# Kernel optimization log

Hardware: AMD Instinct MI355X
Metric: run time of the kernel (lower is better)

## Reference

```python
import jax, jax.numpy as jnp
import numpy as np

N, CIN, C, L = 6144, 6, 128, 3
SIGMA = 0.3

def _ln(x, g, b, eps=1e-5):
    m = x.mean(-1, keepdims=True)
    v = x.var(-1, keepdims=True)
    return (x - m) / jnp.sqrt(v + eps) * g + b

def _cdist(a):
    n2 = jnp.sum(a * a, -1)
    d2 = n2[:, None] + n2[None, :] - 2.0 * (a @ a.T)
    return jnp.sqrt(jnp.maximum(d2, 0.0))

def setup_inputs():
    key = jax.random.key(0)
    ks = jax.random.split(key, 24)
    s = 1.0 / np.sqrt(C)
    ref = jax.random.normal(ks[0], (N, 3), dtype=jnp.float32)
    src = ref + 0.05 * jax.random.normal(ks[1], (N, 3), dtype=jnp.float32)
    return {
        "ref_keypts": ref,
        "src_keypts": src,
        "corr_feat": jax.random.normal(ks[2], (N, CIN), dtype=jnp.float32),
        "W_in": jax.random.normal(ks[3], (CIN + 6, C), dtype=jnp.float32) * (1.0 / np.sqrt(CIN + 6)),
        "b_in": jnp.zeros((C,), jnp.float32),
        "mlp_W": jax.random.normal(ks[4], (L, C, C), dtype=jnp.float32) * s,
        "mlp_b": jnp.zeros((L, C), jnp.float32),
        "mlp_g": jnp.ones((L, C), jnp.float32),
        "mlp_beta": jnp.zeros((L, C), jnp.float32),
        "Wq": jax.random.normal(ks[5], (L, C, C), dtype=jnp.float32) * s,
        "bq": jnp.zeros((L, C), jnp.float32),
        "Wk": jax.random.normal(ks[6], (L, C, C), dtype=jnp.float32) * s,
        "bk": jnp.zeros((L, C), jnp.float32),
        "Wv": jax.random.normal(ks[7], (L, C, C), dtype=jnp.float32) * s,
        "bv": jnp.zeros((L, C), jnp.float32),
        "Wo": jax.random.normal(ks[8], (L, C, C), dtype=jnp.float32) * s,
        "bo": jnp.zeros((L, C), jnp.float32),
        "ln_g": jnp.ones((L, C), jnp.float32),
        "ln_b": jnp.zeros((L, C), jnp.float32),
        "c1_W": jax.random.normal(ks[9], (C, 32), dtype=jnp.float32) * s,
        "c1_b": jnp.zeros((32,), jnp.float32),
        "c2_W": jax.random.normal(ks[10], (32, 32), dtype=jnp.float32) * (1.0 / np.sqrt(32)),
        "c2_b": jnp.zeros((32,), jnp.float32),
        "c3_W": jax.random.normal(ks[11], (32, 1), dtype=jnp.float32) * (1.0 / np.sqrt(32)),
        "c3_b": jnp.zeros((1,), jnp.float32),
    }

def reference(ref_keypts, src_keypts, corr_feat, W_in, b_in, mlp_W, mlp_b, mlp_g, mlp_beta, Wq, bq, Wk, bk, Wv, bv, Wo, bo, ln_g, ln_b, c1_W, c1_b, c2_W, c2_b, c3_W, c3_b):
    # keypoint-diff embedding
    kp = jnp.concatenate([ref_keypts, src_keypts], -1)          # [N, 6]
    kp = kp - kp.mean(-1, keepdims=True)
    feat = jnp.concatenate([corr_feat, kp], -1) @ W_in + b_in   # [N, C]
    # geometric compatibility (no grad in original -> stop_gradient)
    geo = _cdist(ref_keypts) - _cdist(src_keypts)               # [N, N]
    geo = jnp.maximum(1.0 - geo * geo / (SIGMA * SIGMA), 0.0)
    geo = jax.lax.stop_gradient(geo)
    scale = 1.0 / np.sqrt(C)
    for i in range(L):
        # UnaryBlock: Linear -> norm -> LeakyReLU(0.1)
        h = _ln(feat @ mlp_W[i] + mlp_b[i], mlp_g[i], mlp_beta[i])
        feat = jnp.where(h > 0, h, 0.1 * h)
        # AttentionLayer (1 head) with multiplicative attention_factors
        q = feat @ Wq[i] + bq[i]
        k = feat @ Wk[i] + bk[i]
        v = feat @ Wv[i] + bv[i]
        attn = jax.nn.softmax(geo * ((q @ k.T) * scale), axis=-1)  # [N, N]
        hid = (attn @ v) @ Wo[i] + bo[i]
        feat = _ln(hid + feat, ln_g[i], ln_b[i])
    feat = feat / jnp.maximum(jnp.linalg.norm(feat, axis=-1, keepdims=True), 1e-12)
    h = jax.nn.relu(feat @ c1_W + c1_b)
    h = jax.nn.relu(h @ c2_W + c2_b)
    score = jax.nn.sigmoid(h @ c3_W + c3_b)[:, 0]
    return feat, score
```

## Files before the change

kernel.cpp:

```cpp
#include <hip/hip_runtime.h>
#include <math.h>

#define NPTS 6144
#define CH   128

typedef __attribute__((ext_vector_type(8))) short short8;
typedef __attribute__((ext_vector_type(4))) float f32x4;
typedef __attribute__((ext_vector_type(2))) float f32x2;
typedef __attribute__((ext_vector_type(4))) int   i32x4;

__device__ inline ushort f2bf(float f) {
  union { float f; unsigned u; } v; v.f = f;
  unsigned u = v.u;
  u += 0x7fff + ((u >> 16) & 1);
  return (ushort)(u >> 16);
}

__device__ inline f32x2 splat2(float x) { return (f32x2){x, x}; }

__device__ inline float fsqrt(float x) {
  float r; asm("v_sqrt_f32 %0, %1" : "=v"(r) : "v"(x)); return r;
}
__device__ inline float fexp2(float x) {
  float r; asm("v_exp_f32 %0, %1" : "=v"(r) : "v"(x)); return r;
}
__device__ inline unsigned cvtpk(float a, float b) {
  unsigned r;
  asm("v_cvt_pk_bf16_f32 %0, %1, %2" : "=v"(r) : "v"(a), "v"(b));
  return r;
}

__global__ __launch_bounds__(128) void k_embed(
    const float* __restrict__ refp, const float* __restrict__ srcp,
    const float* __restrict__ cf, const float* __restrict__ Win,
    const float* __restrict__ bin, float* __restrict__ out) {
  const int row = blockIdx.x, j = threadIdx.x;
  __shared__ float inb[12];
  __shared__ float mkp;
  if (j < 6)       inb[j] = cf[row * 6 + j];
  else if (j < 9)  inb[j] = refp[row * 3 + (j - 6)];
  else if (j < 12) inb[j] = srcp[row * 3 + (j - 9)];
  __syncthreads();
  if (j == 0) {
    float s = inb[6] + inb[7] + inb[8] + inb[9] + inb[10] + inb[11];
    mkp = s * (1.0f / 6.0f);
  }
  __syncthreads();
  float acc = bin[j];
  #pragma unroll
  for (int kk = 0; kk < 12; kk++) {
    float x = inb[kk] - (kk >= 6 ? mkp : 0.0f);
    acc = fmaf(x, Win[kk * CH + j], acc);
  }
  out[row * CH + j] = acc;
}

__global__ __launch_bounds__(128) void k_mlp_qkv(
    const float* __restrict__ X, const float* __restrict__ W,
    const float* __restrict__ b, const float* __restrict__ g,
    const float* __restrict__ beta,
    const float* __restrict__ Wq, const float* __restrict__ bq,
    const float* __restrict__ Wk, const float* __restrict__ bk,
    const float* __restrict__ Wv, const float* __restrict__ bv,
    float* __restrict__ T, ushort* __restrict__ Q, ushort* __restrict__ K,
    ushort* __restrict__ Vt) {
  const int j = threadIdx.x;
  const int r0 = blockIdx.x * 4;
  __shared__ float xs[4][CH];
  __shared__ float hs[4][CH];
  __shared__ float red[2][4];
  #pragma unroll
  for (int r = 0; r < 4; r++) xs[r][j] = X[(r0 + r) * CH + j];
  __syncthreads();

  float acc[4];
  const float bj = b[j];
  #pragma unroll
  for (int r = 0; r < 4; r++) acc[r] = bj;
  for (int kk = 0; kk < CH; kk++) {
    float wv_ = W[kk * CH + j];
    #pragma unroll
    for (int r = 0; r < 4; r++) acc[r] = fmaf(xs[r][kk], wv_, acc[r]);
  }
  const int wv2 = j >> 6, ln = j & 63;
  float sum[4];
  #pragma unroll
  for (int r = 0; r < 4; r++) sum[r] = acc[r];
  #pragma unroll
  for (int o = 32; o; o >>= 1) {
    #pragma unroll
    for (int r = 0; r < 4; r++) sum[r] += __shfl_xor(sum[r], o);
  }
  if (ln == 0) {
    #pragma unroll
    for (int r = 0; r < 4; r++) red[wv2][r] = sum[r];
  }
  __syncthreads();
  float dv[4];
  #pragma unroll
  for (int r = 0; r < 4; r++) {
    float mean = (red[0][r] + red[1][r]) * (1.0f / 128.0f);
    dv[r] = acc[r] - mean;
    sum[r] = dv[r] * dv[r];
  }
  #pragma unroll
  for (int o = 32; o; o >>= 1) {
    #pragma unroll
    for (int r = 0; r < 4; r++) sum[r] += __shfl_xor(sum[r], o);
  }
  __syncthreads();
  if (ln == 0) {
    #pragma unroll
    for (int r = 0; r < 4; r++) red[wv2][r] = sum[r];
  }
  __syncthreads();
  const float gj = g[j], betaj = beta[j];
  #pragma unroll
  for (int r = 0; r < 4; r++) {
    float var = (red[0][r] + red[1][r]) * (1.0f / 128.0f);
    float y = dv[r] * rsqrtf(var + 1e-5f) * gj + betaj;
    y = (y > 0.0f) ? y : 0.1f * y;
    T[(r0 + r) * CH + j] = y;
    hs[r][j] = y;
  }
  __syncthreads();

  float aq[4], ak[4], av[4];
  const float bqj = bq[j], bkj = bk[j], bvj = bv[j];
  #pragma unroll
  for (int r = 0; r < 4; r++) { aq[r] = bqj; ak[r] = bkj; av[r] = bvj; }
  for (int kk = 0; kk < CH; kk++) {
    float wq = Wq[kk * CH + j], wk = Wk[kk * CH + j], wv_ = Wv[kk * CH + j];
    #pragma unroll
    for (int r = 0; r < 4; r++) {
      float x = hs[r][kk];
      aq[r] = fmaf(x, wq, aq[r]);
      ak[r] = fmaf(x, wk, ak[r]);
      av[r] = fmaf(x, wv_, av[r]);
    }
  }
  const float scale = 0.12751879524143007f;
  #pragma unroll
  for (int r = 0; r < 4; r++) {
    Q[(r0 + r) * CH + j] = f2bf(aq[r] * scale);
    K[(r0 + r) * CH + j] = f2bf(ak[r]);
  }
  ushort4 vp;
  vp.x = f2bf(av[0]); vp.y = f2bf(av[1]); vp.z = f2bf(av[2]); vp.w = f2bf(av[3]);
  const int w0 = r0 & 63;
  const int pos = (r0 & ~63) + 32 * ((w0 >> 5) & 1) + 8 * ((w0 >> 2) & 3) +
                  4 * ((w0 >> 4) & 1);
  *(ushort4*)(Vt + (size_t)j * NPTS + pos) = vp;
}

__global__ __launch_bounds__(256, 2) void k_attn_mfma(
    const ushort* __restrict__ Q, const ushort* __restrict__ K,
    const ushort* __restrict__ Vt,
    const float* __restrict__ refp, const float* __restrict__ srcp,
    float* __restrict__ Opart, float* __restrict__ ML, int ntiles) {
  const int tid = threadIdx.x;
  const int w = tid >> 6, ln = tid & 63;
  const int l15 = ln & 15, g = ln >> 4;
  const int row0 = blockIdx.x * 128;
  const int seg = blockIdx.y;
  const int t0 = seg * ntiles;

  __shared__ ushort Ks[64][128];
  __shared__ ushort Vs[128][64];
  __shared__ float cs2[6][64];

  int kofs[4], vofs[4];
  size_t kgo[4], vgo[4];
  #pragma unroll
  for (int s = 0; s < 4; s++) {
    int idx = tid + 256 * s;
    int kr = idx >> 4, kc = idx & 15;
    kofs[s] = kr * 256 + (((kc ^ (kr & 7)) << 4));
    kgo[s] = (size_t)kr * CH + kc * 8;
    int vr = idx >> 3, vc = idx & 7;
    vofs[s] = vr * 128 + (((vc ^ (vr & 7)) << 4));
    vgo[s] = (size_t)vr * NPTS + vc * 8;
  }

  short8 kreg[4], vreg[4];
  float cr[6];

  auto issue = [&](int t) {
    #pragma unroll
    for (int s = 0; s < 4; s++) {
      kreg[s] = *(const short8*)(K + (size_t)(t * 64) * CH + kgo[s]);
      vreg[s] = *(const short8*)(Vt + vgo[s] + t * 64);
    }
    if (tid < 64) {
      int gj = t * 64 + tid;
      cr[0] = refp[gj * 3]; cr[1] = refp[gj * 3 + 1]; cr[2] = refp[gj * 3 + 2];
      cr[3] = srcp[gj * 3]; cr[4] = srcp[gj * 3 + 1]; cr[5] = srcp[gj * 3 + 2];
    }
  };

  const int qbase = row0 + 32 * w;
  const int q1 = qbase + l15, q2 = qbase + 16 + l15;
  short8 qfA[4], qfB[4];
  {
    const ushort* qpA = Q + (size_t)q1 * CH + 8 * g;
    const ushort* qpB = Q + (size_t)q2 * CH + 8 * g;
    #pragma unroll
    for (int ks = 0; ks < 4; ks++) {
      qfA[ks] = *(const short8*)(qpA + 32 * ks);
      qfB[ks] = *(const short8*)(qpB + 32 * ks);
    }
  }
  const float rq10 = refp[q1 * 3], rq11 = refp[q1 * 3 + 1], rq12 = refp[q1 * 3 + 2];
  const float sq10 = srcp[q1 * 3], sq11 = srcp[q1 * 3 + 1], sq12 = srcp[q1 * 3 + 2];
  const float rq20 = refp[q2 * 3], rq21 = refp[q2 * 3 + 1], rq22 = refp[q2 * 3 + 2];
  const float sq20 = srcp[q2 * 3], sq21 = srcp[q2 * 3 + 1], sq22 = srcp[q2 * 3 + 2];

  f32x4 oA[8], oB[8];
  #pragma unroll
  for (int n = 0; n < 8; n++) {
    oA[n] = (f32x4){0.f, 0.f, 0.f, 0.f};
    oB[n] = (f32x4){0.f, 0.f, 0.f, 0.f};
  }
  float m1 = -1e30f, l1 = 0.0f, m2 = -1e30f, l2 = 0.0f;
  const float invs2 = 1.0f / (0.3f * 0.3f);

  issue(t0);
  #pragma unroll
  for (int s = 0; s < 4; s++) {
    *(short8*)((char*)&Ks[0][0] + kofs[s]) = kreg[s];
    *(short8*)((char*)&Vs[0][0] + vofs[s]) = vreg[s];
  }
  if (tid < 64) {
    #pragma unroll
    for (int d = 0; d < 6; d++) cs2[d][tid] = cr[d];
  }
  __syncthreads();

  for (int tt = 0; tt < ntiles; tt++) {
    if (tt + 1 < ntiles) issue(t0 + tt + 1);

    f32x4 accA[4], accB[4];
    #pragma unroll
    for (int nb = 0; nb < 4; nb++) {
      accA[nb] = (f32x4){0.f, 0.f, 0.f, 0.f};
      accB[nb] = (f32x4){0.f, 0.f, 0.f, 0.f};
    }
    __builtin_amdgcn_s_setprio(1);
    #pragma unroll
    for (int ks = 0; ks < 4; ks++) {
      #pragma unroll
      for (int nb = 0; nb < 4; nb++) {
        const char* src = (const char*)&Ks[0][0] + (16 * nb + l15) * 256 +
                          (((4 * ks + g) ^ (l15 & 7)) << 4);
        short8 af = *(const short8*)src;
        accA[nb] = __builtin_amdgcn_mfma_f32_16x16x32_bf16(af, qfA[ks], accA[nb], 0, 0, 0);
        accB[nb] = __builtin_amdgcn_mfma_f32_16x16x32_bf16(af, qfB[ks], accB[nb], 0, 0, 0);
      }
    }
    __builtin_amdgcn_s_setprio(0);

    float pA[4][4], pB[4][4];
    #pragma unroll
    for (int nb = 0; nb < 4; nb++) {
      const int kb = 16 * nb + 4 * g;
      #pragma unroll
      for (int pp = 0; pp < 2; pp++) {
        const int k2 = kb + 2 * pp;
        f32x2 cx = *(const f32x2*)&cs2[0][k2];
        f32x2 cy = *(const f32x2*)&cs2[1][k2];
        f32x2 cz = *(const f32x2*)&cs2[2][k2];
        f32x2 sx = *(const f32x2*)&cs2[3][k2];
        f32x2 sy = *(const f32x2*)&cs2[4][k2];
        f32x2 sz = *(const f32x2*)&cs2[5][k2];
        {
          f32x2 dx = splat2(rq10) - cx, dy = splat2(rq11) - cy, dz = splat2(rq12) - cz;
          f32x2 d2r = dx * dx + dy * dy + dz * dz;
          dx = splat2(sq10) - sx; dy = splat2(sq11) - sy; dz = splat2(sq12) - sz;
          f32x2 d2s = dx * dx + dy * dy + dz * dz;
          f32x2 prod = d2r * d2s, sum2 = d2r + d2s;
          float s0 = fsqrt(prod[0]), s1 = fsqrt(prod[1]);
          float dd20 = fmaf(-2.0f, s0, sum2[0]);
          float dd21 = fmaf(-2.0f, s1, sum2[1]);
          float gg0 = fmaxf(fmaf(dd20, -invs2, 1.0f), 0.0f);
          float gg1 = fmaxf(fmaf(dd21, -invs2, 1.0f), 0.0f);
          pA[nb][2 * pp]     = gg0 * accA[nb][2 * pp];
          pA[nb][2 * pp + 1] = gg1 * accA[nb][2 * pp + 1];
        }
        {
          f32x2 dx = splat2(rq20) - cx, dy = splat2(rq21) - cy, dz = splat2(rq22) - cz;
          f32x2 d2r = dx * dx + dy * dy + dz * dz;
          dx = splat2(sq20) - sx; dy = splat2(sq21) - sy; dz = splat2(sq22) - sz;
          f32x2 d2s = dx * dx + dy * dy + dz * dz;
          f32x2 prod = d2r * d2s, sum2 = d2r + d2s;
          float s0 = fsqrt(prod[0]), s1 = fsqrt(prod[1]);
          float dd20 = fmaf(-2.0f, s0, sum2[0]);
          float dd21 = fmaf(-2.0f, s1, sum2[1]);
          float gg0 = fmaxf(fmaf(dd20, -invs2, 1.0f), 0.0f);
          float gg1 = fmaxf(fmaf(dd21, -invs2, 1.0f), 0.0f);
          pB[nb][2 * pp]     = gg0 * accB[nb][2 * pp];
          pB[nb][2 * pp + 1] = gg1 * accB[nb][2 * pp + 1];
        }
      }
    }

    float tm1 = pA[0][0], tm2 = pB[0][0];
    #pragma unroll
    for (int nb = 0; nb < 4; nb++)
      #pragma unroll
      for (int r = 0; r < 4; r++) {
        tm1 = fmaxf(tm1, pA[nb][r]);
        tm2 = fmaxf(tm2, pB[nb][r]);
      }
    tm1 = fmaxf(tm1, __shfl_xor(tm1, 16));
    tm1 = fmaxf(tm1, __shfl_xor(tm1, 32));
    tm2 = fmaxf(tm2, __shfl_xor(tm2, 16));
    tm2 = fmaxf(tm2, __shfl_xor(tm2, 32));
    if (__any((tm1 > m1 + 11.0f) || (tm2 > m2 + 11.0f))) {
      float nm1 = fmaxf(m1, tm1), nm2 = fmaxf(m2, tm2);
      float rs1 = fexp2(m1 - nm1), rs2 = fexp2(m2 - nm2);
      l1 *= rs1; l2 *= rs2;
      #pragma unroll
      for (int n = 0; n < 8; n++) { oA[n] *= rs1; oB[n] *= rs2; }
      m1 = nm1; m2 = nm2;
    }
    float ps1 = 0.0f, ps2 = 0.0f;
    #pragma unroll
    for (int nb = 0; nb < 4; nb++)
      #pragma unroll
      for (int r = 0; r < 4; r++) {
        float a = fexp2(pA[nb][r] - m1);
        float b2 = fexp2(pB[nb][r] - m2);
        pA[nb][r] = a; pB[nb][r] = b2;
        ps1 += a; ps2 += b2;
      }
    ps1 += __shfl_xor(ps1, 16); ps1 += __shfl_xor(ps1, 32);
    ps2 += __shfl_xor(ps2, 16); ps2 += __shfl_xor(ps2, 32);
    l1 += ps1; l2 += ps2;

    unsigned pkA[4][2], pkB[4][2];
    #pragma unroll
    for (int nb = 0; nb < 4; nb++) {
      pkA[nb][0] = cvtpk(pA[nb][0], pA[nb][1]);
      pkA[nb][1] = cvtpk(pA[nb][2], pA[nb][3]);
      pkB[nb][0] = cvtpk(pB[nb][0], pB[nb][1]);
      pkB[nb][1] = cvtpk(pB[nb][2], pB[nb][3]);
    }

    __syncthreads();

    if (tt + 1 < ntiles) {
      #pragma unroll
      for (int s = 0; s < 4; s++)
        *(short8*)((char*)&Ks[0][0] + kofs[s]) = kreg[s];
      if (tid < 64) {
        #pragma unroll
        for (int d = 0; d < 6; d++) cs2[d][tid] = cr[d];
      }
    }

    union U16 { i32x4 i; short8 s; };
    __builtin_amdgcn_s_setprio(1);
    #pragma unroll
    for (int ks2 = 0; ks2 < 2; ks2++) {
      U16 bfA, bfB;
      bfA.i[0] = (int)pkA[2 * ks2][0];
      bfA.i[1] = (int)pkA[2 * ks2][1];
      bfA.i[2] = (int)pkA[2 * ks2 + 1][0];
      bfA.i[3] = (int)pkA[2 * ks2 + 1][1];
      bfB.i[0] = (int)pkB[2 * ks2][0];
      bfB.i[1] = (int)pkB[2 * ks2][1];
      bfB.i[2] = (int)pkB[2 * ks2 + 1][0];
      bfB.i[3] = (int)pkB[2 * ks2 + 1][1];
      #pragma unroll
      for (int nb2 = 0; nb2 < 8; nb2++) {
        const char* vsrc = (const char*)&Vs[0][0] + (16 * nb2 + l15) * 128 +
                           (((4 * ks2 + g) ^ (l15 & 7)) << 4);
        short8 vf = *(const short8*)vsrc;
        oA[nb2] = __builtin_amdgcn_mfma_f32_16x16x32_bf16(vf, bfA.s, oA[nb2], 0, 0, 0);
        oB[nb2] = __builtin_amdgcn_mfma_f32_16x16x32_bf16(vf, bfB.s, oB[nb2], 0, 0, 0);
      }
    }
    __builtin_amdgcn_s_setprio(0);

    __syncthreads();

    if (tt + 1 < ntiles) {
      #pragma unroll
      for (int s = 0; s < 4; s++)
        *(short8*)((char*)&Vs[0][0] + vofs[s]) = vreg[s];
    }
  }

  {
    float* op1 = Opart + ((size_t)seg * NPTS + q1) * CH;
    float* op2 = Opart + ((size_t)seg * NPTS + q2) * CH;
    #pragma unroll
    for (int nb2 = 0; nb2 < 8; nb2++) {
      *(f32x4*)(op1 + 16 * nb2 + 4 * g) = oA[nb2];
      *(f32x4*)(op2 + 16 * nb2 + 4 * g) = oB[nb2];
    }
    if (g == 0) {
      ML[((size_t)seg * NPTS + q1) * 2]     = m1;
      ML[((size_t)seg * NPTS + q1) * 2 + 1] = l1;
      ML[((size_t)seg * NPTS + q2) * 2]     = m2;
      ML[((size_t)seg * NPTS + q2) * 2 + 1] = l2;
    }
  }
}

__global__ __launch_bounds__(128) void k_out(
    const float* __restrict__ Opart, const float* __restrict__ ML, int NS,
    const float* __restrict__ W, const float* __restrict__ b,
    const float* __restrict__ g, const float* __restrict__ beta,
    const float* __restrict__ res, float* __restrict__ out) {
  const int j = threadIdx.x;
  const int r0 = blockIdx.x * 4;
  __shared__ float xs[4][CH];
  __shared__ float red[2][4];

  #pragma unroll
  for (int r = 0; r < 4; r++) {
    const int row = r0 + r;
    float M = -1e30f;
    for (int s = 0; s < NS; s++)
      M = fmaxf(M, ML[((size_t)s * NPTS + row) * 2]);
    float L = 0.0f, a = 0.0f;
    for (int s = 0; s < NS; s++) {
      float ms = ML[((size_t)s * NPTS + row) * 2];
      float ls = ML[((size_t)s * NPTS + row) * 2 + 1];
      float wsc = fexp2(ms - M);
      L += wsc * ls;
      a = fmaf(wsc, Opart[((size_t)s * NPTS + row) * CH + j], a);
    }
    xs[r][j] = a / L;
  }
  __syncthreads();

  float acc[4];
  const float bj = b[j];
  #pragma unroll
  for (int r = 0; r < 4; r++) acc[r] = bj;
  for (int kk = 0; kk < CH; kk++) {
    float wv_ = W[kk * CH + j];
    #pragma unroll
    for (int r = 0; r < 4; r++) acc[r] = fmaf(xs[r][kk], wv_, acc[r]);
  }
  #pragma unroll
  for (int r = 0; r < 4; r++) acc[r] += res[(r0 + r) * CH + j];

  const int wv2 = j >> 6, ln = j & 63;
  float sum[4];
  #pragma unroll
  for (int r = 0; r < 4; r++) sum[r] = acc[r];
  #pragma unroll
  for (int o = 32; o; o >>= 1) {
    #pragma unroll
    for (int r = 0; r < 4; r++) sum[r] += __shfl_xor(sum[r], o);
  }
  if (ln == 0) {
    #pragma unroll
    for (int r = 0; r < 4; r++) red[wv2][r] = sum[r];
  }
  __syncthreads();
  float dv[4];
  #pragma unroll
  for (int r = 0; r < 4; r++) {
    float mean = (red[0][r] + red[1][r]) * (1.0f / 128.0f);
    dv[r] = acc[r] - mean;
    sum[r] = dv[r] * dv[r];
  }
  #pragma unroll
  for (int o = 32; o; o >>= 1) {
    #pragma unroll
    for (int r = 0; r < 4; r++) sum[r] += __shfl_xor(sum[r], o);
  }
  __syncthreads();
  if (ln == 0) {
    #pragma unroll
    for (int r = 0; r < 4; r++) red[wv2][r] = sum[r];
  }
  __syncthreads();
  const float gj = g[j], betaj = beta[j];
  #pragma unroll
  for (int r = 0; r < 4; r++) {
    float var = (red[0][r] + red[1][r]) * (1.0f / 128.0f);
    out[(r0 + r) * CH + j] = dv[r] * rsqrtf(var + 1e-5f) * gj + betaj;
  }
}

__global__ __launch_bounds__(128) void k_final(
    const float* __restrict__ F,
    const float* __restrict__ c1W, const float* __restrict__ c1b,
    const float* __restrict__ c2W, const float* __restrict__ c2b,
    const float* __restrict__ c3W, const float* __restrict__ c3b,
    float* __restrict__ out) {
  const int row = blockIdx.x, j = threadIdx.x;
  __shared__ float xs[CH];
  __shared__ float h1[32];
  __shared__ float h2[32];
  __shared__ float red[2];
  float x = F[row * CH + j];
  float ss = x * x;
  #pragma unroll
  for (int o = 32; o; o >>= 1) ss += __shfl_xor(ss, o);
  if ((j & 63) == 0) red[j >> 6] = ss;
  __syncthreads();
  float norm = sqrtf(red[0] + red[1]);
  float xn = x / fmaxf(norm, 1e-12f);
  xs[j] = xn;
  out[row * CH + j] = xn;
  __syncthreads();
  if (j < 32) {
    float a = c1b[j];
    for (int kk = 0; kk < CH; kk++) a = fmaf(xs[kk], c1W[kk * 32 + j], a);
    h1[j] = fmaxf(a, 0.0f);
  }
  __syncthreads();
  if (j < 32) {
    float a = c2b[j];
    #pragma unroll
    for (int kk = 0; kk < 32; kk++) a = fmaf(h1[kk], c2W[kk * 32 + j], a);
    h2[j] = fmaxf(a, 0.0f);
  }
  __syncthreads();
  if (j == 0) {
    float a = c3b[0];
    #pragma unroll
    for (int kk = 0; kk < 32; kk++) a = fmaf(h2[kk], c3W[kk], a);
    out[NPTS * CH + row] = 1.0f / (1.0f + __expf(-a));
  }
}

extern "C" void kernel_launch(void* const* d_in, const int* in_sizes, int n_in,
                              void* d_out, int out_size, void* d_ws, size_t ws_size,
                              hipStream_t stream) {
  const float* refp = (const float*)d_in[0];
  const float* srcp = (const float*)d_in[1];
  const float* cf   = (const float*)d_in[2];
  const float* Win  = (const float*)d_in[3];
  const float* bin  = (const float*)d_in[4];
  const float* mlpW = (const float*)d_in[5];
  const float* mlpb = (const float*)d_in[6];
  const float* mlpg = (const float*)d_in[7];
  const float* mlpbeta = (const float*)d_in[8];
  const float* Wq = (const float*)d_in[9];
  const float* bq = (const float*)d_in[10];
  const float* Wk = (const float*)d_in[11];
  const float* bk = (const float*)d_in[12];
  const float* Wv = (const float*)d_in[13];
  const float* bv = (const float*)d_in[14];
  const float* Wo = (const float*)d_in[15];
  const float* bo = (const float*)d_in[16];
  const float* lng = (const float*)d_in[17];
  const float* lnb = (const float*)d_in[18];
  const float* c1W = (const float*)d_in[19];
  const float* c1b = (const float*)d_in[20];
  const float* c2W = (const float*)d_in[21];
  const float* c2b = (const float*)d_in[22];
  const float* c3W = (const float*)d_in[23];
  const float* c3b = (const float*)d_in[24];
  float* out = (float*)d_out;

  const size_t NC = (size_t)NPTS * CH;
  const size_t seg_bytes = NC * 4 + (size_t)NPTS * 8;
  const size_t base = 2 * NC * 4 + 3 * NC * 2;

  int NS = 1;
  {
    const int cands[8] = {16, 12, 8, 6, 4, 3, 2, 1};
    for (int i = 0; i < 8; i++)
      if (base + (size_t)cands[i] * seg_bytes <= ws_size) { NS = cands[i]; break; }
  }

  char* p = (char*)d_ws;
  float* F = (float*)p;        p += NC * 4;
  float* T = (float*)p;        p += NC * 4;
  ushort* Qb = (ushort*)p;     p += NC * 2;
  ushort* Kb = (ushort*)p;     p += NC * 2;
  ushort* Vtb = (ushort*)p;    p += NC * 2;
  float* Opart = (float*)p;    p += (size_t)NS * NC * 4;
  float* ML = (float*)p;
  const int ntiles = NPTS / 64 / NS;

  k_embed<<<NPTS, 128, 0, stream>>>(refp, srcp, cf, Win, bin, F);
  for (int i = 0; i < 3; i++) {
    const int o2 = i * CH * CH, o1 = i * CH;
    k_mlp_qkv<<<NPTS / 4, 128, 0, stream>>>(
        F, mlpW + o2, mlpb + o1, mlpg + o1, mlpbeta + o1,
        Wq + o2, bq + o1, Wk + o2, bk + o1, Wv + o2, bv + o1,
        T, Qb, Kb, Vtb);
    dim3 agrid(NPTS / 128, NS);
    k_attn_mfma<<<agrid, 256, 0, stream>>>(Qb, Kb, Vtb, refp, srcp,
                                           Opart, ML, ntiles);
    k_out<<<NPTS / 4, 128, 0, stream>>>(Opart, ML, NS, Wo + o2, bo + o1,
                                        lng + o1, lnb + o1, T, F);
  }
  k_final<<<NPTS, 128, 0, stream>>>(F, c1W, c1b, c2W, c2b, c3W, c3b, out);
}
```

Baseline: 394.4 us.

## Precompute geometric compatibility matrix once in fp16 and store attention partials as bf16

Adds a kernel that computes the N×N geometric compatibility matrix once, stored in fp16 in the workspace when it fits. The three attention layers then read it instead of recomputing distances and square roots per tile. Partial attention outputs are also written as bf16 instead of fp32 to cut traffic between the attention and output kernels. The trade is roughly 75 MB of extra geo reads per layer against the saved VALU work, plus some precision loss in geo and the partials.

Result: faster. 356.6 us (-9.6%).

```diff
diff --git a/kernel.cpp b/kernel.cpp
--- a/kernel.cpp
+++ b/kernel.cpp
@@ -8,6 +8,7 @@
 typedef __attribute__((ext_vector_type(4))) float f32x4;
 typedef __attribute__((ext_vector_type(2))) float f32x2;
 typedef __attribute__((ext_vector_type(4))) int   i32x4;
+typedef __attribute__((ext_vector_type(2))) unsigned u32x2;
 
 __device__ inline ushort f2bf(float f) {
   union { float f; unsigned u; } v; v.f = f;
@@ -15,6 +16,9 @@
   u += 0x7fff + ((u >> 16) & 1);
   return (ushort)(u >> 16);
 }
+__device__ inline float bf2f(ushort h) {
+  union { unsigned u; float f; } v; v.u = ((unsigned)h) << 16; return v.f;
+}
 
 __device__ inline f32x2 splat2(float x) { return (f32x2){x, x}; }
 
@@ -28,6 +32,46 @@
   unsigned r;
   asm("v_cvt_pk_bf16_f32 %0, %1, %2" : "=v"(r) : "v"(a), "v"(b));
   return r;
+}
+__device__ inline float h2f(ushort h) {
+  float r; asm("v_cvt_f32_f16 %0, %1" : "=v"(r) : "v"((unsigned)h)); return r;
+}
+__device__ inline ushort f2h(float f) {
+  unsigned r; asm("v_cvt_f16_f32 %0, %1" : "=v"(r) : "v"(f)); return (ushort)r;
+}
+
+__global__ __launch_bounds__(256) void k_geo(
+    const float* __restrict__ refp, const float* __restrict__ srcp,
+    ushort* __restrict__ geo) {
+  const int tid = threadIdx.x;
+  const int w = tid >> 6, ln = tid & 63;
+  const int q = blockIdx.x * 4 + w;
+  __shared__ float kco[6][256];
+  const float rq0 = refp[q * 3], rq1 = refp[q * 3 + 1], rq2 = refp[q * 3 + 2];
+  const float sq0 = srcp[q * 3], sq1 = srcp[q * 3 + 1], sq2 = srcp[q * 3 + 2];
+  const float invs2 = 1.0f / (0.3f * 0.3f);
+  for (int kb = 0; kb < NPTS / 256; kb++) {
+    __syncthreads();
+    {
+      int k = kb * 256 + tid;
+      kco[0][tid] = refp[k * 3]; kco[1][tid] = refp[k * 3 + 1];
+      kco[2][tid] = refp[k * 3 + 2];
+      kco[3][tid] = srcp[k * 3]; kco[4][tid] = srcp[k * 3 + 1];
+      kco[5][tid] = srcp[k * 3 + 2];
+    }
+    __syncthreads();
+    #pragma unroll
+    for (int i = 0; i < 4; i++) {
+      int kl = ln + 64 * i;
+      float dx = rq0 - kco[0][kl], dy = rq1 - kco[1][kl], dz = rq2 - kco[2][kl];
+      float d2r = dx * dx + dy * dy + dz * dz;
+      dx = sq0 - kco[3][kl]; dy = sq1 - kco[4][kl]; dz = sq2 - kco[5][kl];
+      float d2s = dx * dx + dy * dy + dz * dz;
+      float dd2 = fmaf(-2.0f, fsqrt(d2r * d2s), d2r + d2s);
+      float gg = fmaxf(fmaf(dd2, -invs2, 1.0f), 0.0f);
+      geo[(size_t)q * NPTS + kb * 256 + kl] = f2h(gg);
+    }
+  }
 }
 
 __global__ __launch_bounds__(128) void k_embed(
@@ -153,11 +197,12 @@
   *(ushort4*)(Vt + (size_t)j * NPTS + pos) = vp;
 }
 
+template <int GEO>
 __global__ __launch_bounds__(256, 2) void k_attn_mfma(
     const ushort* __restrict__ Q, const ushort* __restrict__ K,
-    const ushort* __restrict__ Vt,
+    const ushort* __restrict__ Vt, const ushort* __restrict__ geo,
     const float* __restrict__ refp, const float* __restrict__ srcp,
-    float* __restrict__ Opart, float* __restrict__ ML, int ntiles) {
+    ushort* __restrict__ Opart, float* __restrict__ ML, int ntiles) {
   const int tid = threadIdx.x;
   const int w = tid >> 6, ln = tid & 63;
   const int l15 = ln & 15, g = ln >> 4;
@@ -167,7 +212,7 @@
 
   __shared__ ushort Ks[64][128];
   __shared__ ushort Vs[128][64];
-  __shared__ float cs2[6][64];
+  __shared__ float cs2[6][(GEO == 0) ? 64 : 4];
 
   int kofs[4], vofs[4];
   size_t kgo[4], vgo[4];
@@ -191,10 +236,12 @@
       kreg[s] = *(const short8*)(K + (size_t)(t * 64) * CH + kgo[s]);
       vreg[s] = *(const short8*)(Vt + vgo[s] + t * 64);
     }
-    if (tid < 64) {
-      int gj = t * 64 + tid;
-      cr[0] = refp[gj * 3]; cr[1] = refp[gj * 3 + 1]; cr[2] = refp[gj * 3 + 2];
-      cr[3] = srcp[gj * 3]; cr[4] = srcp[gj * 3 + 1]; cr[5] = srcp[gj * 3 + 2];
+    if constexpr (GEO == 0) {
+      if (tid < 64) {
+        int gj = t * 64 + tid;
+        cr[0] = refp[gj * 3]; cr[1] = refp[gj * 3 + 1]; cr[2] = refp[gj * 3 + 2];
+        cr[3] = srcp[gj * 3]; cr[4] = srcp[gj * 3 + 1]; cr[5] = srcp[gj * 3 + 2];
+      }
     }
   };
 
@@ -210,10 +257,14 @@
       qfB[ks] = *(const short8*)(qpB + 32 * ks);
     }
   }
-  const float rq10 = refp[q1 * 3], rq11 = refp[q1 * 3 + 1], rq12 = refp[q1 * 3 + 2];
-  const float sq10 = srcp[q1 * 3], sq11 = srcp[q1 * 3 + 1], sq12 = srcp[q1 * 3 + 2];
-  const float rq20 = refp[q2 * 3], rq21 = refp[q2 * 3 + 1], rq22 = refp[q2 * 3 + 2];
-  const float sq20 = srcp[q2 * 3], sq21 = srcp[q2 * 3 + 1], sq22 = srcp[q2 * 3 + 2];
+  float rq10 = 0, rq11 = 0, rq12 = 0, sq10 = 0, sq11 = 0, sq12 = 0;
+  float rq20 = 0, rq21 = 0, rq22 = 0, sq20 = 0, sq21 = 0, sq22 = 0;
+  if constexpr (GEO == 0) {
+    rq10 = refp[q1 * 3]; rq11 = refp[q1 * 3 + 1]; rq12 = refp[q1 * 3 + 2];
+    sq10 = srcp[q1 * 3]; sq11 = srcp[q1 * 3 + 1]; sq12 = srcp[q1 * 3 + 2];
+    rq20 = refp[q2 * 3]; rq21 = refp[q2 * 3 + 1]; rq22 = refp[q2 * 3 + 2];
+    sq20 = srcp[q2 * 3]; sq21 = srcp[q2 * 3 + 1]; sq22 = srcp[q2 * 3 + 2];
+  }
 
   f32x4 oA[8], oB[8];
   #pragma unroll
@@ -230,14 +281,28 @@
     *(short8*)((char*)&Ks[0][0] + kofs[s]) = kreg[s];
     *(short8*)((char*)&Vs[0][0] + vofs[s]) = vreg[s];
   }
-  if (tid < 64) {
-    #pragma unroll
-    for (int d = 0; d < 6; d++) cs2[d][tid] = cr[d];
+  if constexpr (GEO == 0) {
+    if (tid < 64) {
+      #pragma unroll
+      for (int d = 0; d < 6; d++) cs2[d][tid] = cr[d];
+    }
   }
   __syncthreads();
 
   for (int tt = 0; tt < ntiles; tt++) {
-    if (tt + 1 < ntiles) issue(t0 + tt + 1);
+    const int t = t0 + tt;
+    if (tt + 1 < ntiles) issue(t + 1);
+
+    ushort4 gA[4], gB[4];
+    if constexpr (GEO == 1) {
+      const ushort* gp1 = geo + (size_t)q1 * NPTS + t * 64 + 4 * g;
+      const ushort* gp2 = geo + (size_t)q2 * NPTS + t * 64 + 4 * g;
+      #pragma unroll
+      for (int nb = 0; nb < 4; nb++) {
+        gA[nb] = *(const ushort4*)(gp1 + 16 * nb);
+        gB[nb] = *(const ushort4*)(gp2 + 16 * nb);
+      }
+    }
 
     f32x4 accA[4], accB[4];
     #pragma unroll
@@ -260,45 +325,59 @@
     __builtin_amdgcn_s_setprio(0);
 
     float pA[4][4], pB[4][4];
-    #pragma unroll
-    for (int nb = 0; nb < 4; nb++) {
-      const int kb = 16 * nb + 4 * g;
-      #pragma unroll
-      for (int pp = 0; pp < 2; pp++) {
-        const int k2 = kb + 2 * pp;
-        f32x2 cx = *(const f32x2*)&cs2[0][k2];
-        f32x2 cy = *(const f32x2*)&cs2[1][k2];
-        f32x2 cz = *(const f32x2*)&cs2[2][k2];
-        f32x2 sx = *(const f32x2*)&cs2[3][k2];
-        f32x2 sy = *(const f32x2*)&cs2[4][k2];
-        f32x2 sz = *(const f32x2*)&cs2[5][k2];
-        {
-          f32x2 dx = splat2(rq10) - cx, dy = splat2(rq11) - cy, dz = splat2(rq12) - cz;
-          f32x2 d2r = dx * dx + dy * dy + dz * dz;
-          dx = splat2(sq10) - sx; dy = splat2(sq11) - sy; dz = splat2(sq12) - sz;
-          f32x2 d2s = dx * dx + dy * dy + dz * dz;
-          f32x2 prod = d2r * d2s, sum2 = d2r + d2s;
-          float s0 = fsqrt(prod[0]), s1 = fsqrt(prod[1]);
-          float dd20 = fmaf(-2.0f, s0, sum2[0]);
-          float dd21 = fmaf(-2.0f, s1, sum2[1]);
-          float gg0 = fmaxf(fmaf(dd20, -invs2, 1.0f), 0.0f);
-          float gg1 = fmaxf(fmaf(dd21, -invs2, 1.0f), 0.0f);
-          pA[nb][2 * pp]     = gg0 * accA[nb][2 * pp];
-          pA[nb][2 * pp + 1] = gg1 * accA[nb][2 * pp + 1];
-        }
-        {
-          f32x2 dx = splat2(rq20) - cx, dy = splat2(rq21) - cy, dz = splat2(rq22) - cz;
-          f32x2 d2r = dx * dx + dy * dy + dz * dz;
-          dx = splat2(sq20) - sx; dy = splat2(sq21) - sy; dz = splat2(sq22) - sz;
-          f32x2 d2s = dx * dx + dy * dy + dz * dz;
-          f32x2 prod = d2r * d2s, sum2 = d2r + d2s;
-          float s0 = fsqrt(prod[0]), s1 = fsqrt(prod[1]);
-          float dd20 = fmaf(-2.0f, s0, sum2[0]);
-          float dd21 = fmaf(-2.0f, s1, sum2[1]);
-          float gg0 = fmaxf(fmaf(dd20, -invs2, 1.0f), 0.0f);
-          float gg1 = fmaxf(fmaf(dd21, -invs2, 1.0f), 0.0f);
-          pB[nb][2 * pp]     = gg0 * accB[nb][2 * pp];
-          pB[nb][2 * pp + 1] = gg1 * accB[nb][2 * pp + 1];
+    if constexpr (GEO == 1) {
+      #pragma unroll
+      for (int nb = 0; nb < 4; nb++) {
+        pA[nb][0] = h2f(gA[nb].x) * accA[nb][0];
+        pA[nb][1] = h2f(gA[nb].y) * accA[nb][1];
+        pA[nb][2] = h2f(gA[nb].z) * accA[nb][2];
+        pA[nb][3] = h2f(gA[nb].w) * accA[nb][3];
+        pB[nb][0] = h2f(gB[nb].x) * accB[nb][0];
+        pB[nb][1] = h2f(gB[nb].y) * accB[nb][1];
+        pB[nb][2] = h2f(gB[nb].z) * accB[nb][2];
+        pB[nb][3] = h2f(gB[nb].w) * accB[nb][3];
+      }
+    } else {
+      #pragma unroll
+      for (int nb = 0; nb < 4; nb++) {
+        const int kb = 16 * nb + 4 * g;
+        #pragma unroll
+        for (int pp = 0; pp < 2; pp++) {
+          const int k2 = kb + 2 * pp;
+          f32x2 cx = *(const f32x2*)&cs2[0][k2];
+          f32x2 cy = *(const f32x2*)&cs2[1][k2];
+          f32x2 cz = *(const f32x2*)&cs2[2][k2];
+          f32x2 sx = *(const f32x2*)&cs2[3][k2];
+          f32x2 sy = *(const f32x2*)&cs2[4][k2];
+          f32x2 sz = *(const f32x2*)&cs2[5][k2];
+          {
+            f32x2 dx = splat2(rq10) - cx, dy = splat2(rq11) - cy, dz = splat2(rq12) - cz;
+            f32x2 d2r = dx * dx + dy * dy + dz * dz;
+            dx = splat2(sq10) - sx; dy = splat2(sq11) - sy; dz = splat2(sq12) - sz;
+            f32x2 d2s = dx * dx + dy * dy + dz * dz;
+            f32x2 prod = d2r * d2s, sum2 = d2r + d2s;
+            float s0 = fsqrt(prod[0]), s1 = fsqrt(prod[1]);
+            float dd20 = fmaf(-2.0f, s0, sum2[0]);
+            float dd21 = fmaf(-2.0f, s1, sum2[1]);
+            float gg0 = fmaxf(fmaf(dd20, -invs2, 1.0f), 0.0f);
+            float gg1 = fmaxf(fmaf(dd21, -invs2, 1.0f), 0.0f);
+            pA[nb][2 * pp]     = gg0 * accA[nb][2 * pp];
+            pA[nb][2 * pp + 1] = gg1 * accA[nb][2 * pp + 1];
+          }
+          {
+            f32x2 dx = splat2(rq20) - cx, dy = splat2(rq21) - cy, dz = splat2(rq22) - cz;
+            f32x2 d2r = dx * dx + dy * dy + dz * dz;
+            dx = splat2(sq20) - sx; dy = splat2(sq21) - sy; dz = splat2(sq22) - sz;
+            f32x2 d2s = dx * dx + dy * dy + dz * dz;
+            f32x2 prod = d2r * d2s, sum2 = d2r + d2s;
+            float s0 = fsqrt(prod[0]), s1 = fsqrt(prod[1]);
+            float dd20 = fmaf(-2.0f, s0, sum2[0]);
+            float dd21 = fmaf(-2.0f, s1, sum2[1]);
+            float gg0 = fmaxf(fmaf(dd20, -invs2, 1.0f), 0.0f);
+            float gg1 = fmaxf(fmaf(dd21, -invs2, 1.0f), 0.0f);
+            pB[nb][2 * pp]     = gg0 * accB[nb][2 * pp];
+            pB[nb][2 * pp + 1] = gg1 * accB[nb][2 * pp + 1];
+          }
         }
       }
     }
@@ -352,9 +431,11 @@
       #pragma unroll
       for (int s = 0; s < 4; s++)
         *(short8*)((char*)&Ks[0][0] + kofs[s]) = kreg[s];
-      if (tid < 64) {
-        #pragma unroll
-        for (int d = 0; d < 6; d++) cs2[d][tid] = cr[d];
+      if constexpr (GEO == 0) {
+        if (tid < 64) {
+          #pragma unroll
+          for (int d = 0; d < 6; d++) cs2[d][tid] = cr[d];
+        }
       }
     }
 
@@ -392,12 +473,17 @@
   }
 
   {
-    float* op1 = Opart + ((size_t)seg * NPTS + q1) * CH;
-    float* op2 = Opart + ((size_t)seg * NPTS + q2) * CH;
+    ushort* op1 = Opart + ((size_t)seg * NPTS + q1) * CH;
+    ushort* op2 = Opart + ((size_t)seg * NPTS + q2) * CH;
     #pragma unroll
     for (int nb2 = 0; nb2 < 8; nb2++) {
-      *(f32x4*)(op1 + 16 * nb2 + 4 * g) = oA[nb2];
-      *(f32x4*)(op2 + 16 * nb2 + 4 * g) = oB[nb2];
+      u32x2 a, b2;
+      a[0] = cvtpk(oA[nb2][0], oA[nb2][1]);
+      a[1] = cvtpk(oA[nb2][2], oA[nb2][3]);
+      b2[0] = cvtpk(oB[nb2][0], oB[nb2][1]);
+      b2[1] = cvtpk(oB[nb2][2], oB[nb2][3]);
+      *(u32x2*)(op1 + 16 * nb2 + 4 * g) = a;
+      *(u32x2*)(op2 + 16 * nb2 + 4 * g) = b2;
     }
     if (g == 0) {
       ML[((size_t)seg * NPTS + q1) * 2]     = m1;
@@ -409,7 +495,7 @@
 }
 
 __global__ __launch_bounds__(128) void k_out(
-    const float* __restrict__ Opart, const float* __restrict__ ML, int NS,
+    const ushort* __restrict__ Opart, const float* __restrict__ ML, int NS,
     const float* __restrict__ W, const float* __restrict__ b,
     const float* __restrict__ g, const float* __restrict__ beta,
     const float* __restrict__ res, float* __restrict__ out) {
@@ -430,7 +516,7 @@
       float ls = ML[((size_t)s * NPTS + row) * 2 + 1];
       float wsc = fexp2(ms - M);
       L += wsc * ls;
-      a = fmaf(wsc, Opart[((size_t)s * NPTS + row) * CH + j], a);
+      a = fmaf(wsc, bf2f(Opart[((size_t)s * NPTS + row) * CH + j]), a);
     }
     xs[r][j] = a / L;
   }
@@ -562,14 +648,23 @@
   float* out = (float*)d_out;
 
   const size_t NC = (size_t)NPTS * CH;
-  const size_t seg_bytes = NC * 4 + (size_t)NPTS * 8;
+  const size_t geo_bytes = (size_t)NPTS * NPTS * 2;
+  const size_t seg_bytes = NC * 2 + (size_t)NPTS * 8;
   const size_t base = 2 * NC * 4 + 3 * NC * 2;
 
-  int NS = 1;
+  int NS = 0;
+  bool useGeo = false;
   {
     const int cands[8] = {16, 12, 8, 6, 4, 3, 2, 1};
     for (int i = 0; i < 8; i++)
-      if (base + (size_t)cands[i] * seg_bytes <= ws_size) { NS = cands[i]; break; }
+      if (base + geo_bytes + (size_t)cands[i] * seg_bytes <= ws_size) {
+        NS = cands[i]; useGeo = true; break;
+      }
+    if (!NS) {
+      for (int i = 0; i < 8; i++)
+        if (base + (size_t)cands[i] * seg_bytes <= ws_size) { NS = cands[i]; break; }
+      if (!NS) NS = 1;
+    }
   }
 
   char* p = (char*)d_ws;
@@ -578,10 +673,14 @@
   ushort* Qb = (ushort*)p;     p += NC * 2;
   ushort* Kb = (ushort*)p;     p += NC * 2;
   ushort* Vtb = (ushort*)p;    p += NC * 2;
-  float* Opart = (float*)p;    p += (size_t)NS * NC * 4;
+  ushort* geo = nullptr;
+  if (useGeo) { geo = (ushort*)p; p += geo_bytes; }
+  ushort* Opart = (ushort*)p;  p += (size_t)NS * NC * 2;
   float* ML = (float*)p;
   const int ntiles = NPTS / 64 / NS;
 
+  if (useGeo)
+    k_geo<<<NPTS / 4, 256, 0, stream>>>(refp, srcp, geo);
   k_embed<<<NPTS, 128, 0, stream>>>(refp, srcp, cf, Win, bin, F);
   for (int i = 0; i < 3; i++) {
     const int o2 = i * CH * CH, o1 = i * CH;
@@ -590,8 +689,12 @@
         Wq + o2, bq + o1, Wk + o2, bk + o1, Wv + o2, bv + o1,
         T, Qb, Kb, Vtb);
     dim3 agrid(NPTS / 128, NS);
-    k_attn_mfma<<<agrid, 256, 0, stream>>>(Qb, Kb, Vtb, refp, srcp,
-                                           Opart, ML, ntiles);
+    if (useGeo)
+      k_attn_mfma<1><<<agrid, 256, 0, stream>>>(Qb, Kb, Vtb, geo, refp, srcp,
+                                                Opart, ML, ntiles);
+    else
+      k_attn_mfma<0><<<agrid, 256, 0, stream>>>(Qb, Kb, Vtb, nullptr, refp, srcp,
+                                                Opart, ML, ntiles);
     k_out<<<NPTS / 4, 128, 0, stream>>>(Opart, ML, NS, Wo + o2, bo + o1,
                                         lng + o1, lnb + o1, T, F);
   }
```
